# Optimization experiments

Measured on AMD Instinct MI355X. Metric: run time of the kernel, lower is better.

## Reference

```python
import jax, jax.numpy as jnp
import numpy as np
import math

B, T, D = 2, 2048, 1024
H = 16
DH = D // H
DFF = 4096
EPS = 1e-5


def setup_inputs() -> dict:
    key = jax.random.key(0)
    ks = jax.random.split(key, 10)
    x = jax.random.normal(ks[0], (B, T, D), dtype=jnp.float32)
    # bool mask, True above diagonal => masked (matches masked_fill semantics)
    causal_mask = jnp.triu(jnp.ones((T, T), dtype=bool), k=1)
    s = 0.02
    return {
        "x": x,
        "causal_mask": causal_mask,
        "gamma1": jnp.ones((D,), jnp.float32),
        "beta1": jnp.zeros((D,), jnp.float32),
        "wq": jax.random.normal(ks[1], (D, D), jnp.float32) * s,
        "wk": jax.random.normal(ks[2], (D, D), jnp.float32) * s,
        "wv": jax.random.normal(ks[3], (D, D), jnp.float32) * s,
        "wo": jax.random.normal(ks[4], (D, D), jnp.float32) * s,
        "gamma2": jnp.ones((D,), jnp.float32),
        "beta2": jnp.zeros((D,), jnp.float32),
        "w1": jax.random.normal(ks[5], (D, DFF), jnp.float32) * s,
        "b1": jnp.zeros((DFF,), jnp.float32),
        "w2": jax.random.normal(ks[6], (DFF, D), jnp.float32) * s,
        "b2": jnp.zeros((D,), jnp.float32),
    }


def _layer_norm(x, gamma, beta):
    mean = jnp.mean(x, axis=-1, keepdims=True)
    var = jnp.mean((x - mean) ** 2, axis=-1, keepdims=True)
    xhat = (x - mean) / jnp.sqrt(var + EPS)
    return gamma * xhat + beta


def _split_heads(x):
    b, t, d = x.shape
    return x.reshape(b, t, H, DH).transpose(0, 2, 1, 3)  # (B,H,T,Dh)


def reference(x, causal_mask, gamma1, beta1, wq, wk, wv, wo,
              gamma2, beta2, w1, b1, w2, b2):
    # --- attention sublayer (pre-LN) ---
    h = _layer_norm(x, gamma1, beta1)
    q = _split_heads(h @ wq)
    k = _split_heads(h @ wk)
    v = _split_heads(h @ wv)
    scores = jnp.einsum('bhqd,bhkd->bhqk', q, k) / math.sqrt(DH)  # (B,H,T,T)
    scores = jnp.where(causal_mask[None, None, :, :], -jnp.inf, scores)
    attn = jax.nn.softmax(scores, axis=-1)
    out = jnp.einsum('bhqk,bhkd->bhqd', attn, v)
    out = out.transpose(0, 2, 1, 3).reshape(x.shape)  # merge heads
    attn_out = out @ wo
    x = x + attn_out
    # --- FFN sublayer (pre-LN) ---
    h = _layer_norm(x, gamma2, beta2)
    ffn = jax.nn.gelu(h @ w1 + b1, approximate=False) @ w2 + b2
    return x + ffn
```

## Files before the change

kernel.cpp:

```cpp
#include <hip/hip_runtime.h>
#include <hip/hip_bf16.h>
#include <math.h>

#define B_   2
#define T_   2048
#define D_   1024
#define H_   16
#define DH_  64
#define DFF_ 4096
#define NTOK (B_*T_)

typedef __attribute__((ext_vector_type(8))) short short8;
typedef __attribute__((ext_vector_type(4))) float f32x4;

static __device__ __forceinline__ short f2bf(float f) {
    union { __hip_bfloat16 h; short s; } u;
    u.h = __float2bfloat16(f);
    return u.s;
}

static __device__ __forceinline__ f32x4 mfma16(short8 a, short8 b, f32x4 c) {
    return __builtin_amdgcn_mfma_f32_16x16x32_bf16(a, b, c, 0, 0, 0);
}

static __device__ __forceinline__ void gload16(const void* g, void* l) {
    __builtin_amdgcn_global_load_lds(
        (__attribute__((address_space(1))) void*)g,
        (__attribute__((address_space(3))) void*)l, 16, 0, 0);
}

static __device__ __forceinline__ short8 lds_read_sw(const short* base, int row, int kbyte) {
    const int off = (row << 7) + (kbyte ^ ((row & 7) << 4));
    return *reinterpret_cast<const short8*>(reinterpret_cast<const char*>(base) + off);
}

__global__ __launch_bounds__(256) void transpose_cast(
    const float* __restrict__ src, short* __restrict__ dst, int K, int N, float scale)
{
    __shared__ short tile[32][33];
    const int k0 = blockIdx.y * 32, n0 = blockIdx.x * 32;
    const int tx = threadIdx.x, ty = threadIdx.y;
    #pragma unroll
    for (int j = 0; j < 4; ++j) {
        int k = ty + j * 8;
        tile[k][tx] = f2bf(src[(size_t)(k0 + k) * N + n0 + tx] * scale);
    }
    __syncthreads();
    #pragma unroll
    for (int j = 0; j < 4; ++j) {
        int n = ty + j * 8;
        dst[(size_t)(n0 + n) * K + k0 + tx] = tile[tx][n];
    }
}

__global__ __launch_bounds__(256) void ln_kernel(
    const float* __restrict__ in, const float* __restrict__ gamma,
    const float* __restrict__ beta, short* __restrict__ out)
{
    const int row = blockIdx.x;
    const int t = threadIdx.x;
    const float4 v = *reinterpret_cast<const float4*>(in + (size_t)row * D_ + t * 4);
    float s  = v.x + v.y + v.z + v.w;
    float sq = v.x*v.x + v.y*v.y + v.z*v.z + v.w*v.w;
    #pragma unroll
    for (int off = 32; off >= 1; off >>= 1) {
        s  += __shfl_xor(s, off);
        sq += __shfl_xor(sq, off);
    }
    __shared__ float ps[4], pq[4];
    if ((t & 63) == 0) { ps[t >> 6] = s; pq[t >> 6] = sq; }
    __syncthreads();
    s  = ps[0] + ps[1] + ps[2] + ps[3];
    sq = pq[0] + pq[1] + pq[2] + pq[3];
    const float mean = s * (1.0f / D_);
    float var = sq * (1.0f / D_) - mean * mean;
    var = fmaxf(var, 0.0f);
    const float rstd = rsqrtf(var + 1e-5f);
    const float4 g = *reinterpret_cast<const float4*>(gamma + t * 4);
    const float4 b = *reinterpret_cast<const float4*>(beta  + t * 4);
    short4 o;
    o.x = f2bf(g.x * ((v.x - mean) * rstd) + b.x);
    o.y = f2bf(g.y * ((v.y - mean) * rstd) + b.y);
    o.z = f2bf(g.z * ((v.z - mean) * rstd) + b.z);
    o.w = f2bf(g.w * ((v.w - mean) * rstd) + b.w);
    *reinterpret_cast<short4*>(out + (size_t)row * D_ + t * 4) = o;
}

template<int BM, int BN, int WR, int WC, int EPI>
__global__ __launch_bounds__(256) void gemm_kernel(
    const short* __restrict__ A, const short* __restrict__ Bt,
    void* __restrict__ Cout, const float* __restrict__ resid,
    const float* __restrict__ bias, int M, int N, int K, int nbx)
{
    constexpr int MB = BM / WR / 16;
    constexpr int NB = BN / WC / 16;
    constexpr int JA = BM / 32;
    constexpr int JB = BN / 32;
    __shared__ short As[2][BM * 64];
    __shared__ short Bs[2][BN * 64];
    const int t = threadIdx.x;
    const int wid = t >> 6, lane = t & 63;
    const int lr = lane & 15, lk = lane >> 4;
    const int cpx = (int)gridDim.x >> 3;
    const int bid = (int)blockIdx.x;
    const int swz = (bid & 7) * cpx + (bid >> 3);
    const int m0 = (swz / nbx) * BM, n0 = (swz % nbx) * BN;
    const int wrow = (wid / WC) * (BM / WR);
    const int wcol = (wid % WC) * (BN / WC);

    const char* aSrc[JA];
    const char* bSrc[JB];
    #pragma unroll
    for (int j = 0; j < JA; ++j) {
        const int off = j * 4096 + t * 16;
        const int r   = off >> 7;
        const int cb  = (off & 127) ^ ((r & 7) << 4);
        aSrc[j] = (const char*)(A + (size_t)(m0 + r) * K) + cb;
    }
    #pragma unroll
    for (int j = 0; j < JB; ++j) {
        const int off = j * 4096 + t * 16;
        const int r   = off >> 7;
        const int cb  = (off & 127) ^ ((r & 7) << 4);
        bSrc[j] = (const char*)(Bt + (size_t)(n0 + r) * K) + cb;
    }

    f32x4 acc[MB][NB];
    #pragma unroll
    for (int m = 0; m < MB; ++m)
        #pragma unroll
        for (int n = 0; n < NB; ++n) acc[m][n] = (f32x4){0.f, 0.f, 0.f, 0.f};

    const int NT = K >> 6;

    #pragma unroll
    for (int j = 0; j < JA; ++j)
        gload16(aSrc[j], (char*)As[0] + j * 4096 + wid * 1024);
    #pragma unroll
    for (int j = 0; j < JB; ++j)
        gload16(bSrc[j], (char*)Bs[0] + j * 4096 + wid * 1024);
    __syncthreads();

    int cur = 0;
    for (int kt = 0; kt < NT; ++kt) {
        if (kt + 1 < NT) {
            const int kb = (kt + 1) << 7;
            #pragma unroll
            for (int j = 0; j < JA; ++j)
                gload16(aSrc[j] + kb, (char*)As[cur ^ 1] + j * 4096 + wid * 1024);
            #pragma unroll
            for (int j = 0; j < JB; ++j)
                gload16(bSrc[j] + kb, (char*)Bs[cur ^ 1] + j * 4096 + wid * 1024);
        }
        #pragma unroll
        for (int kk = 0; kk < 64; kk += 32) {
            short8 af[MB], bf[NB];
            #pragma unroll
            for (int m = 0; m < MB; ++m)
                af[m] = lds_read_sw(As[cur], wrow + m * 16 + lr, (kk + lk * 8) * 2);
            #pragma unroll
            for (int n = 0; n < NB; ++n)
                bf[n] = lds_read_sw(Bs[cur], wcol + n * 16 + lr, (kk + lk * 8) * 2);
            #pragma unroll
            for (int m = 0; m < MB; ++m)
                #pragma unroll
                for (int n = 0; n < NB; ++n)
                    acc[m][n] = mfma16(af[m], bf[n], acc[m][n]);
        }
        __syncthreads();
        cur ^= 1;
    }

    #pragma unroll
    for (int m = 0; m < MB; ++m) {
        #pragma unroll
        for (int n = 0; n < NB; ++n) {
            #pragma unroll
            for (int r = 0; r < 4; ++r) {
                const int gr = m0 + wrow + m * 16 + lk * 4 + r;
                const int gc = n0 + wcol + n * 16 + lr;
                const size_t idx = (size_t)gr * N + gc;
                const float v = acc[m][n][r];
                if constexpr (EPI == 0) {
                    ((short*)Cout)[idx] = f2bf(v);
                } else if constexpr (EPI == 1) {
                    ((float*)Cout)[idx] = resid[idx] + v;
                } else if constexpr (EPI == 2) {
                    const float tt = v + bias[gc];
                    const float ge = 0.5f * tt * (1.0f + erff(tt * 0.70710678118654752f));
                    ((short*)Cout)[idx] = f2bf(ge);
                } else {
                    ((float*)Cout)[idx] = resid[idx] + v + bias[gc];
                }
            }
        }
    }
}

__global__ __launch_bounds__(512) void vtrans(
    const short* __restrict__ qkv, short* __restrict__ vT)
{
    __shared__ short tile[64][65];
    const int qt = blockIdx.x;
    const int bh = blockIdx.y;
    const int b = bh >> 4, h = bh & 15;
    const int tx = threadIdx.x, ty = threadIdx.y;
    const short* src = qkv + ((size_t)(b * T_ + qt * 64)) * 3072 + 2048 + h * 64;
    #pragma unroll
    for (int j = 0; j < 8; ++j) {
        int tl = ty + j * 8;
        tile[tl][tx] = src[(size_t)tl * 3072 + tx];
    }
    __syncthreads();
    short* dst = vT + ((size_t)bh * 64) * T_ + qt * 64;
    #pragma unroll
    for (int j = 0; j < 8; ++j) {
        int dh = ty + j * 8;
        dst[(size_t)dh * T_ + tx] = tile[tx][dh];
    }
}

__global__ __launch_bounds__(256) void attn_kernel(
    const short* __restrict__ qkv, const short* __restrict__ vT,
    short* __restrict__ attn)
{
    __shared__ short Ks[2][4096];
    __shared__ short Vs[2][4096];
    __shared__ short Ps[4][1024];
    const int xx = blockIdx.x;
    const int bh = blockIdx.y;
    const int a  = xx & 7, bq = xx >> 3;
    const int i2 = ((bh >> 3) + bq) & 3;
    const int qt = (i2 == 0) ? a : (i2 == 1) ? 31 - a : (i2 == 2) ? 8 + a : 23 - a;
    const int b = bh >> 4, h = bh & 15;
    const int t = threadIdx.x;
    const int wid = t >> 6, lane = t & 63;
    const int lr = lane & 15, lk = lane >> 4;
    const int q0 = qt * 64 + wid * 16;

    const short* qrow = qkv + (size_t)(b * T_ + q0 + lr) * 3072 + h * 64;
    const short8 qf0 = *reinterpret_cast<const short8*>(qrow + lk * 8);
    const short8 qf1 = *reinterpret_cast<const short8*>(qrow + 32 + lk * 8);
    const short* kbase = qkv + (size_t)b * T_ * 3072 + 1024 + h * 64;
    const short* vbase = vT + (size_t)bh * 64 * T_;

    f32x4 o[4];
    float mr[4], lsp[4];
    #pragma unroll
    for (int n = 0; n < 4; ++n) o[n] = (f32x4){0.f, 0.f, 0.f, 0.f};
    #pragma unroll
    for (int r = 0; r < 4; ++r) { mr[r] = -INFINITY; lsp[r] = 0.f; }

    const int nkt = qt + 1;

    #pragma unroll
    for (int j = 0; j < 2; ++j) {
        const int off = j * 4096 + t * 16;
        const int r   = off >> 7;
        const int cb  = (off & 127) ^ ((r & 7) << 4);
        gload16(kbase + (size_t)r * 3072 + (cb >> 1), (char*)Ks[0] + j * 4096 + wid * 1024);
        gload16(vbase + (size_t)r * T_   + (cb >> 1), (char*)Vs[0] + j * 4096 + wid * 1024);
    }
    __syncthreads();

    int cur = 0;
    for (int kt = 0; kt < nkt; ++kt) {
        const int kvb = kt * 64;
        if (kt + 1 < nkt) {
            const int nb = kvb + 64;
            #pragma unroll
            for (int j = 0; j < 2; ++j) {
                const int off = j * 4096 + t * 16;
                const int r   = off >> 7;
                const int cb  = (off & 127) ^ ((r & 7) << 4);
                gload16(kbase + (size_t)(nb + r) * 3072 + (cb >> 1),
                        (char*)Ks[cur ^ 1] + j * 4096 + wid * 1024);
                gload16(vbase + (size_t)r * T_ + nb + (cb >> 1),
                        (char*)Vs[cur ^ 1] + j * 4096 + wid * 1024);
            }
        }

        f32x4 s[4];
        #pragma unroll
        for (int n = 0; n < 4; ++n) s[n] = (f32x4){0.f, 0.f, 0.f, 0.f};
        #pragma unroll
        for (int n = 0; n < 4; ++n) {
            s[n] = mfma16(qf0, lds_read_sw(Ks[cur], n * 16 + lr, (lk * 8) * 2), s[n]);
            s[n] = mfma16(qf1, lds_read_sw(Ks[cur], n * 16 + lr, (32 + lk * 8) * 2), s[n]);
        }

        const bool needmask = (kt == qt);
        char* pw = (char*)&Ps[wid][0];
        #pragma unroll
        for (int r = 0; r < 4; ++r) {
            const int qg = q0 + lk * 4 + r;
            float v0 = s[0][r], v1 = s[1][r], v2 = s[2][r], v3 = s[3][r];
            if (needmask) {
                if (kvb +      lr > qg) v0 = -INFINITY;
                if (kvb + 16 + lr > qg) v1 = -INFINITY;
                if (kvb + 32 + lr > qg) v2 = -INFINITY;
                if (kvb + 48 + lr > qg) v3 = -INFINITY;
            }
            const float mxl = fmaxf(fmaxf(v0, v1), fmaxf(v2, v3));
            if (!__all(mxl <= mr[r] + 8.0f)) {
                float mx = mxl;
                mx = fmaxf(mx, __shfl_xor(mx, 1));
                mx = fmaxf(mx, __shfl_xor(mx, 2));
                mx = fmaxf(mx, __shfl_xor(mx, 4));
                mx = fmaxf(mx, __shfl_xor(mx, 8));
                const float mnew = fmaxf(mr[r], mx);
                const float alpha = __builtin_amdgcn_exp2f(mr[r] - mnew);
                o[0][r] *= alpha; o[1][r] *= alpha; o[2][r] *= alpha; o[3][r] *= alpha;
                lsp[r] *= alpha;
                mr[r] = mnew;
            }
            const float p0 = __builtin_amdgcn_exp2f(v0 - mr[r]);
            const float p1 = __builtin_amdgcn_exp2f(v1 - mr[r]);
            const float p2 = __builtin_amdgcn_exp2f(v2 - mr[r]);
            const float p3 = __builtin_amdgcn_exp2f(v3 - mr[r]);
            lsp[r] += p0 + p1 + p2 + p3;
            const int prow = lk * 4 + r;
            const int sw = (prow & 7) << 4;
            char* prb = pw + prow * 128;
            *(short*)(prb + (((     lr * 2)) ^ sw)) = f2bf(p0);
            *(short*)(prb + ((32 + lr * 2) ^ sw)) = f2bf(p1);
            *(short*)(prb + ((64 + lr * 2) ^ sw)) = f2bf(p2);
            *(short*)(prb + ((96 + lr * 2) ^ sw)) = f2bf(p3);
        }
        asm volatile("s_waitcnt lgkmcnt(0)" ::: "memory");

        #pragma unroll
        for (int kk = 0; kk < 2; ++kk) {
            const short8 pf = *reinterpret_cast<const short8*>(
                pw + lr * 128 + ((kk * 64 + lk * 16) ^ ((lr & 7) << 4)));
            #pragma unroll
            for (int n = 0; n < 4; ++n)
                o[n] = mfma16(pf, lds_read_sw(Vs[cur], n * 16 + lr, (kk * 32 + lk * 8) * 2), o[n]);
        }
        __syncthreads();
        cur ^= 1;
    }

    #pragma unroll
    for (int r = 0; r < 4; ++r) {
        float l = lsp[r];
        l += __shfl_xor(l, 1);
        l += __shfl_xor(l, 2);
        l += __shfl_xor(l, 4);
        l += __shfl_xor(l, 8);
        const float inv = 1.0f / l;
        short* op = attn + (size_t)(b * T_ + q0 + lk * 4 + r) * D_ + h * 64;
        #pragma unroll
        for (int n = 0; n < 4; ++n)
            op[n * 16 + lr] = f2bf(o[n][r] * inv);
    }
}

extern "C" void kernel_launch(void* const* d_in, const int* in_sizes, int n_in,
                              void* d_out, int out_size, void* d_ws, size_t ws_size,
                              hipStream_t stream)
{
    (void)in_sizes; (void)n_in; (void)out_size; (void)ws_size;
    const float* x      = (const float*)d_in[0];
    const float* gamma1 = (const float*)d_in[2];
    const float* beta1  = (const float*)d_in[3];
    const float* wq     = (const float*)d_in[4];
    const float* wk     = (const float*)d_in[5];
    const float* wv     = (const float*)d_in[6];
    const float* wo     = (const float*)d_in[7];
    const float* gamma2 = (const float*)d_in[8];
    const float* beta2  = (const float*)d_in[9];
    const float* w1     = (const float*)d_in[10];
    const float* b1     = (const float*)d_in[11];
    const float* w2     = (const float*)d_in[12];
    const float* b2     = (const float*)d_in[13];
    float* out = (float*)d_out;

    char* ws = (char*)d_ws;
    size_t off = 0;
    short* wqkvT = (short*)(ws + off); off += (size_t)3072 * 1024 * 2;
    short* woT   = (short*)(ws + off); off += (size_t)1024 * 1024 * 2;
    short* w1T   = (short*)(ws + off); off += (size_t)4096 * 1024 * 2;
    short* w2T   = (short*)(ws + off); off += (size_t)1024 * 4096 * 2;
    short* h1    = (short*)(ws + off); off += (size_t)NTOK * 1024 * 2;
    short* h2    = (short*)(ws + off); off += (size_t)NTOK * 1024 * 2;
    float* y     = (float*)(ws + off); off += (size_t)NTOK * 1024 * 4;
    short* attnb = (short*)(ws + off); off += (size_t)NTOK * 1024 * 2;
    short* qkv   = (short*)(ws + off); off += (size_t)NTOK * 3072 * 2;
    short* vT    = (short*)(ws + off); off += (size_t)B_ * H_ * DH_ * T_ * 2;
    short* g     = qkv;

    const dim3 tb(32, 8);
    transpose_cast<<<dim3(32, 32),  tb, 0, stream>>>(wq, wqkvT,               1024, 1024, 0.18033688011112042f);
    transpose_cast<<<dim3(32, 32),  tb, 0, stream>>>(wk, wqkvT + 1024 * 1024, 1024, 1024, 1.0f);
    transpose_cast<<<dim3(32, 32),  tb, 0, stream>>>(wv, wqkvT + 2048 * 1024, 1024, 1024, 1.0f);
    transpose_cast<<<dim3(32, 32),  tb, 0, stream>>>(wo, woT,                 1024, 1024, 1.0f);
    transpose_cast<<<dim3(128, 32), tb, 0, stream>>>(w1, w1T, 1024, 4096, 1.0f);
    transpose_cast<<<dim3(32, 128), tb, 0, stream>>>(w2, w2T, 4096, 1024, 1.0f);

    ln_kernel<<<NTOK, 256, 0, stream>>>(x, gamma1, beta1, h1);

    gemm_kernel<128, 128, 2, 2, 0><<<768, 256, 0, stream>>>(
        h1, wqkvT, qkv, nullptr, nullptr, NTOK, 3072, 1024, 24);

    vtrans<<<dim3(T_ / 64, B_ * H_), dim3(64, 8), 0, stream>>>(qkv, vT);

    attn_kernel<<<dim3(T_ / 64, B_ * H_), 256, 0, stream>>>(qkv, vT, attnb);

    gemm_kernel<128, 64, 2, 2, 1><<<512, 256, 0, stream>>>(
        attnb, woT, y, x, nullptr, NTOK, 1024, 1024, 16);

    ln_kernel<<<NTOK, 256, 0, stream>>>(y, gamma2, beta2, h2);

    gemm_kernel<128, 128, 2, 2, 2><<<1024, 256, 0, stream>>>(
        h2, w1T, g, nullptr, b1, NTOK, 4096, 1024, 32);

    gemm_kernel<128, 64, 2, 2, 3><<<512, 256, 0, stream>>>(
        g, w2T, out, y, b2, NTOK, 1024, 4096, 16);
}
```

Before: 271.7 us.

## Fuse V-transpose into QKV GEMM, pair causal q-tiles, widen GEMM blocks

```diff
diff --git a/kernel.cpp b/kernel.cpp
--- a/kernel.cpp
+++ b/kernel.cpp
@@ -86,16 +86,17 @@
     *reinterpret_cast<short4*>(out + (size_t)row * D_ + t * 4) = o;
 }
 
-template<int BM, int BN, int WR, int WC, int EPI>
-__global__ __launch_bounds__(256) void gemm_kernel(
+template<int BM, int BN, int EPI>
+__global__ __launch_bounds__(512) void gemm_kernel(
     const short* __restrict__ A, const short* __restrict__ Bt,
     void* __restrict__ Cout, const float* __restrict__ resid,
-    const float* __restrict__ bias, int M, int N, int K, int nbx)
-{
-    constexpr int MB = BM / WR / 16;
-    constexpr int NB = BN / WC / 16;
-    constexpr int JA = BM / 32;
-    constexpr int JB = BN / 32;
+    const float* __restrict__ bias, short* __restrict__ vaux,
+    int M, int N, int K, int nbx)
+{
+    constexpr int MB = BM / 4 / 16;
+    constexpr int NB = BN / 2 / 16;
+    constexpr int JA = BM / 64;
+    constexpr int JB = BN / 64;
     __shared__ short As[2][BM * 64];
     __shared__ short Bs[2][BN * 64];
     const int t = threadIdx.x;
@@ -105,21 +106,21 @@
     const int bid = (int)blockIdx.x;
     const int swz = (bid & 7) * cpx + (bid >> 3);
     const int m0 = (swz / nbx) * BM, n0 = (swz % nbx) * BN;
-    const int wrow = (wid / WC) * (BM / WR);
-    const int wcol = (wid % WC) * (BN / WC);
+    const int wrow = (wid >> 1) * (BM / 4);
+    const int wcol = (wid & 1) * (BN / 2);
 
     const char* aSrc[JA];
     const char* bSrc[JB];
     #pragma unroll
     for (int j = 0; j < JA; ++j) {
-        const int off = j * 4096 + t * 16;
+        const int off = j * 8192 + t * 16;
         const int r   = off >> 7;
         const int cb  = (off & 127) ^ ((r & 7) << 4);
         aSrc[j] = (const char*)(A + (size_t)(m0 + r) * K) + cb;
     }
     #pragma unroll
     for (int j = 0; j < JB; ++j) {
-        const int off = j * 4096 + t * 16;
+        const int off = j * 8192 + t * 16;
         const int r   = off >> 7;
         const int cb  = (off & 127) ^ ((r & 7) << 4);
         bSrc[j] = (const char*)(Bt + (size_t)(n0 + r) * K) + cb;
@@ -135,10 +136,10 @@
 
     #pragma unroll
     for (int j = 0; j < JA; ++j)
-        gload16(aSrc[j], (char*)As[0] + j * 4096 + wid * 1024);
+        gload16(aSrc[j], (char*)As[0] + j * 8192 + wid * 1024);
     #pragma unroll
     for (int j = 0; j < JB; ++j)
-        gload16(bSrc[j], (char*)Bs[0] + j * 4096 + wid * 1024);
+        gload16(bSrc[j], (char*)Bs[0] + j * 8192 + wid * 1024);
     __syncthreads();
 
     int cur = 0;
@@ -147,10 +148,10 @@
             const int kb = (kt + 1) << 7;
             #pragma unroll
             for (int j = 0; j < JA; ++j)
-                gload16(aSrc[j] + kb, (char*)As[cur ^ 1] + j * 4096 + wid * 1024);
+                gload16(aSrc[j] + kb, (char*)As[cur ^ 1] + j * 8192 + wid * 1024);
             #pragma unroll
             for (int j = 0; j < JB; ++j)
-                gload16(bSrc[j] + kb, (char*)Bs[cur ^ 1] + j * 4096 + wid * 1024);
+                gload16(bSrc[j] + kb, (char*)Bs[cur ^ 1] + j * 8192 + wid * 1024);
         }
         #pragma unroll
         for (int kk = 0; kk < 64; kk += 32) {
@@ -189,34 +190,79 @@
                     const float tt = v + bias[gc];
                     const float ge = 0.5f * tt * (1.0f + erff(tt * 0.70710678118654752f));
                     ((short*)Cout)[idx] = f2bf(ge);
+                } else if constexpr (EPI == 3) {
+                    ((float*)Cout)[idx] = resid[idx] + v + bias[gc];
                 } else {
-                    ((float*)Cout)[idx] = resid[idx] + v + bias[gc];
+                    if (gc < 2048) {
+                        ((short*)Cout)[idx] = f2bf(v);
+                    } else {
+                        const int hh = (gc - 2048) >> 6, dh = (gc - 2048) & 63;
+                        const int bb = gr >> 11, tl = gr & 2047;
+                        vaux[((size_t)((bb << 4) + hh) * 64 + dh) * 2048 + tl] = f2bf(v);
+                    }
                 }
             }
         }
     }
 }
 
-__global__ __launch_bounds__(512) void vtrans(
-    const short* __restrict__ qkv, short* __restrict__ vT)
-{
-    __shared__ short tile[64][65];
-    const int qt = blockIdx.x;
-    const int bh = blockIdx.y;
-    const int b = bh >> 4, h = bh & 15;
-    const int tx = threadIdx.x, ty = threadIdx.y;
-    const short* src = qkv + ((size_t)(b * T_ + qt * 64)) * 3072 + 2048 + h * 64;
-    #pragma unroll
-    for (int j = 0; j < 8; ++j) {
-        int tl = ty + j * 8;
-        tile[tl][tx] = src[(size_t)tl * 3072 + tx];
-    }
-    __syncthreads();
-    short* dst = vT + ((size_t)bh * 64) * T_ + qt * 64;
-    #pragma unroll
-    for (int j = 0; j < 8; ++j) {
-        int dh = ty + j * 8;
-        dst[(size_t)dh * T_ + tx] = tile[tx][dh];
+static __device__ __forceinline__ void attn_tile(
+    const short* Kcur, const short* Vcur, char* pw,
+    short8 qf0, short8 qf1, int q0, int kvb, bool diag,
+    int lr, int lk, f32x4 (&o)[4], float (&mr)[4], float (&ls)[4])
+{
+    f32x4 s[4];
+    #pragma unroll
+    for (int n = 0; n < 4; ++n) s[n] = (f32x4){0.f, 0.f, 0.f, 0.f};
+    #pragma unroll
+    for (int n = 0; n < 4; ++n) {
+        s[n] = mfma16(qf0, lds_read_sw(Kcur, n * 16 + lr, (lk * 8) * 2), s[n]);
+        s[n] = mfma16(qf1, lds_read_sw(Kcur, n * 16 + lr, (32 + lk * 8) * 2), s[n]);
+    }
+    #pragma unroll
+    for (int r = 0; r < 4; ++r) {
+        const int qg = q0 + lk * 4 + r;
+        float v0 = s[0][r], v1 = s[1][r], v2 = s[2][r], v3 = s[3][r];
+        if (diag) {
+            if (kvb +      lr > qg) v0 = -INFINITY;
+            if (kvb + 16 + lr > qg) v1 = -INFINITY;
+            if (kvb + 32 + lr > qg) v2 = -INFINITY;
+            if (kvb + 48 + lr > qg) v3 = -INFINITY;
+        }
+        const float mxl = fmaxf(fmaxf(v0, v1), fmaxf(v2, v3));
+        if (!__all(mxl <= mr[r] + 8.0f)) {
+            float mx = mxl;
+            mx = fmaxf(mx, __shfl_xor(mx, 1));
+            mx = fmaxf(mx, __shfl_xor(mx, 2));
+            mx = fmaxf(mx, __shfl_xor(mx, 4));
+            mx = fmaxf(mx, __shfl_xor(mx, 8));
+            const float mnew = fmaxf(mr[r], mx);
+            const float alpha = __builtin_amdgcn_exp2f(mr[r] - mnew);
+            o[0][r] *= alpha; o[1][r] *= alpha; o[2][r] *= alpha; o[3][r] *= alpha;
+            ls[r] *= alpha;
+            mr[r] = mnew;
+        }
+        const float p0 = __builtin_amdgcn_exp2f(v0 - mr[r]);
+        const float p1 = __builtin_amdgcn_exp2f(v1 - mr[r]);
+        const float p2 = __builtin_amdgcn_exp2f(v2 - mr[r]);
+        const float p3 = __builtin_amdgcn_exp2f(v3 - mr[r]);
+        ls[r] += p0 + p1 + p2 + p3;
+        const int prow = lk * 4 + r;
+        const int sw = (prow & 7) << 4;
+        char* prb = pw + prow * 128;
+        *(short*)(prb + (((     lr * 2)) ^ sw)) = f2bf(p0);
+        *(short*)(prb + ((32 + lr * 2) ^ sw)) = f2bf(p1);
+        *(short*)(prb + ((64 + lr * 2) ^ sw)) = f2bf(p2);
+        *(short*)(prb + ((96 + lr * 2) ^ sw)) = f2bf(p3);
+    }
+    asm volatile("s_waitcnt lgkmcnt(0)" ::: "memory");
+    #pragma unroll
+    for (int kk = 0; kk < 2; ++kk) {
+        const short8 pf = *reinterpret_cast<const short8*>(
+            pw + lr * 128 + ((kk * 64 + lk * 16) ^ ((lr & 7) << 4)));
+        #pragma unroll
+        for (int n = 0; n < 4; ++n)
+            o[n] = mfma16(pf, lds_read_sw((const short*)Vcur, n * 16 + lr, (kk * 32 + lk * 8) * 2), o[n]);
     }
 }
 
@@ -226,32 +272,40 @@
 {
     __shared__ short Ks[2][4096];
     __shared__ short Vs[2][4096];
-    __shared__ short Ps[4][1024];
+    __shared__ short Ps[2][4][1024];
     const int xx = blockIdx.x;
     const int bh = blockIdx.y;
-    const int a  = xx & 7, bq = xx >> 3;
-    const int i2 = ((bh >> 3) + bq) & 3;
-    const int qt = (i2 == 0) ? a : (i2 == 1) ? 31 - a : (i2 == 2) ? 8 + a : 23 - a;
+    const int qA = xx, qB = 31 - xx;
     const int b = bh >> 4, h = bh & 15;
     const int t = threadIdx.x;
     const int wid = t >> 6, lane = t & 63;
     const int lr = lane & 15, lk = lane >> 4;
-    const int q0 = qt * 64 + wid * 16;
-
-    const short* qrow = qkv + (size_t)(b * T_ + q0 + lr) * 3072 + h * 64;
-    const short8 qf0 = *reinterpret_cast<const short8*>(qrow + lk * 8);
-    const short8 qf1 = *reinterpret_cast<const short8*>(qrow + 32 + lk * 8);
+    const int q0A = qA * 64 + wid * 16;
+    const int q0B = qB * 64 + wid * 16;
+
+    const short* qrowA = qkv + (size_t)(b * T_ + q0A + lr) * 3072 + h * 64;
+    const short8 qfA0 = *reinterpret_cast<const short8*>(qrowA + lk * 8);
+    const short8 qfA1 = *reinterpret_cast<const short8*>(qrowA + 32 + lk * 8);
+    const short* qrowB = qkv + (size_t)(b * T_ + q0B + lr) * 3072 + h * 64;
+    const short8 qfB0 = *reinterpret_cast<const short8*>(qrowB + lk * 8);
+    const short8 qfB1 = *reinterpret_cast<const short8*>(qrowB + 32 + lk * 8);
     const short* kbase = qkv + (size_t)b * T_ * 3072 + 1024 + h * 64;
     const short* vbase = vT + (size_t)bh * 64 * T_;
 
-    f32x4 o[4];
-    float mr[4], lsp[4];
-    #pragma unroll
-    for (int n = 0; n < 4; ++n) o[n] = (f32x4){0.f, 0.f, 0.f, 0.f};
-    #pragma unroll
-    for (int r = 0; r < 4; ++r) { mr[r] = -INFINITY; lsp[r] = 0.f; }
-
-    const int nkt = qt + 1;
+    f32x4 oA[4], oB[4];
+    float mrA[4], lsA[4], mrB[4], lsB[4];
+    #pragma unroll
+    for (int n = 0; n < 4; ++n) {
+        oA[n] = (f32x4){0.f, 0.f, 0.f, 0.f};
+        oB[n] = (f32x4){0.f, 0.f, 0.f, 0.f};
+    }
+    #pragma unroll
+    for (int r = 0; r < 4; ++r) {
+        mrA[r] = -INFINITY; lsA[r] = 0.f;
+        mrB[r] = -INFINITY; lsB[r] = 0.f;
+    }
+
+    const int nkt = qB + 1;
 
     #pragma unroll
     for (int j = 0; j < 2; ++j) {
@@ -280,79 +334,31 @@
             }
         }
 
-        f32x4 s[4];
-        #pragma unroll
-        for (int n = 0; n < 4; ++n) s[n] = (f32x4){0.f, 0.f, 0.f, 0.f};
+        attn_tile(Ks[cur], Vs[cur], (char*)&Ps[1][wid][0],
+                  qfB0, qfB1, q0B, kvb, kt == qB, lr, lk, oB, mrB, lsB);
+        if (kt <= qA)
+            attn_tile(Ks[cur], Vs[cur], (char*)&Ps[0][wid][0],
+                      qfA0, qfA1, q0A, kvb, kt == qA, lr, lk, oA, mrA, lsA);
+
+        __syncthreads();
+        cur ^= 1;
+    }
+
+    #pragma unroll
+    for (int r = 0; r < 4; ++r) {
+        float lA = lsA[r], lB = lsB[r];
+        lA += __shfl_xor(lA, 1); lB += __shfl_xor(lB, 1);
+        lA += __shfl_xor(lA, 2); lB += __shfl_xor(lB, 2);
+        lA += __shfl_xor(lA, 4); lB += __shfl_xor(lB, 4);
+        lA += __shfl_xor(lA, 8); lB += __shfl_xor(lB, 8);
+        const float invA = 1.0f / lA, invB = 1.0f / lB;
+        short* opA = attn + (size_t)(b * T_ + q0A + lk * 4 + r) * D_ + h * 64;
+        short* opB = attn + (size_t)(b * T_ + q0B + lk * 4 + r) * D_ + h * 64;
         #pragma unroll
         for (int n = 0; n < 4; ++n) {
-            s[n] = mfma16(qf0, lds_read_sw(Ks[cur], n * 16 + lr, (lk * 8) * 2), s[n]);
-            s[n] = mfma16(qf1, lds_read_sw(Ks[cur], n * 16 + lr, (32 + lk * 8) * 2), s[n]);
-        }
-
-        const bool needmask = (kt == qt);
-        char* pw = (char*)&Ps[wid][0];
-        #pragma unroll
-        for (int r = 0; r < 4; ++r) {
-            const int qg = q0 + lk * 4 + r;
-            float v0 = s[0][r], v1 = s[1][r], v2 = s[2][r], v3 = s[3][r];
-            if (needmask) {
-                if (kvb +      lr > qg) v0 = -INFINITY;
-                if (kvb + 16 + lr > qg) v1 = -INFINITY;
-                if (kvb + 32 + lr > qg) v2 = -INFINITY;
-                if (kvb + 48 + lr > qg) v3 = -INFINITY;
-            }
-            const float mxl = fmaxf(fmaxf(v0, v1), fmaxf(v2, v3));
-            if (!__all(mxl <= mr[r] + 8.0f)) {
-                float mx = mxl;
-                mx = fmaxf(mx, __shfl_xor(mx, 1));
-                mx = fmaxf(mx, __shfl_xor(mx, 2));
-                mx = fmaxf(mx, __shfl_xor(mx, 4));
-                mx = fmaxf(mx, __shfl_xor(mx, 8));
-                const float mnew = fmaxf(mr[r], mx);
-                const float alpha = __builtin_amdgcn_exp2f(mr[r] - mnew);
-                o[0][r] *= alpha; o[1][r] *= alpha; o[2][r] *= alpha; o[3][r] *= alpha;
-                lsp[r] *= alpha;
-                mr[r] = mnew;
-            }
-            const float p0 = __builtin_amdgcn_exp2f(v0 - mr[r]);
-            const float p1 = __builtin_amdgcn_exp2f(v1 - mr[r]);
-            const float p2 = __builtin_amdgcn_exp2f(v2 - mr[r]);
-            const float p3 = __builtin_amdgcn_exp2f(v3 - mr[r]);
-            lsp[r] += p0 + p1 + p2 + p3;
-            const int prow = lk * 4 + r;
-            const int sw = (prow & 7) << 4;
-            char* prb = pw + prow * 128;
-            *(short*)(prb + (((     lr * 2)) ^ sw)) = f2bf(p0);
-            *(short*)(prb + ((32 + lr * 2) ^ sw)) = f2bf(p1);
-            *(short*)(prb + ((64 + lr * 2) ^ sw)) = f2bf(p2);
-            *(short*)(prb + ((96 + lr * 2) ^ sw)) = f2bf(p3);
-        }
-        asm volatile("s_waitcnt lgkmcnt(0)" ::: "memory");
-
-        #pragma unroll
-        for (int kk = 0; kk < 2; ++kk) {
-            const short8 pf = *reinterpret_cast<const short8*>(
-                pw + lr * 128 + ((kk * 64 + lk * 16) ^ ((lr & 7) << 4)));
-            #pragma unroll
-            for (int n = 0; n < 4; ++n)
-                o[n] = mfma16(pf, lds_read_sw(Vs[cur], n * 16 + lr, (kk * 32 + lk * 8) * 2), o[n]);
-        }
-        __syncthreads();
-        cur ^= 1;
-    }
-
-    #pragma unroll
-    for (int r = 0; r < 4; ++r) {
-        float l = lsp[r];
-        l += __shfl_xor(l, 1);
-        l += __shfl_xor(l, 2);
-        l += __shfl_xor(l, 4);
-        l += __shfl_xor(l, 8);
-        const float inv = 1.0f / l;
-        short* op = attn + (size_t)(b * T_ + q0 + lk * 4 + r) * D_ + h * 64;
-        #pragma unroll
-        for (int n = 0; n < 4; ++n)
-            op[n * 16 + lr] = f2bf(o[n][r] * inv);
+            opA[n * 16 + lr] = f2bf(oA[n][r] * invA);
+            opB[n * 16 + lr] = f2bf(oB[n][r] * invB);
+        }
     }
 }
 
@@ -400,21 +406,19 @@
 
     ln_kernel<<<NTOK, 256, 0, stream>>>(x, gamma1, beta1, h1);
 
-    gemm_kernel<128, 128, 2, 2, 0><<<768, 256, 0, stream>>>(
-        h1, wqkvT, qkv, nullptr, nullptr, NTOK, 3072, 1024, 24);
-
-    vtrans<<<dim3(T_ / 64, B_ * H_), dim3(64, 8), 0, stream>>>(qkv, vT);
-
-    attn_kernel<<<dim3(T_ / 64, B_ * H_), 256, 0, stream>>>(qkv, vT, attnb);
-
-    gemm_kernel<128, 64, 2, 2, 1><<<512, 256, 0, stream>>>(
-        attnb, woT, y, x, nullptr, NTOK, 1024, 1024, 16);
+    gemm_kernel<128, 128, 4><<<768, 512, 0, stream>>>(
+        h1, wqkvT, qkv, nullptr, nullptr, vT, NTOK, 3072, 1024, 24);
+
+    attn_kernel<<<dim3(16, 32), 256, 0, stream>>>(qkv, vT, attnb);
+
+    gemm_kernel<128, 64, 1><<<512, 512, 0, stream>>>(
+        attnb, woT, y, x, nullptr, nullptr, NTOK, 1024, 1024, 16);
 
     ln_kernel<<<NTOK, 256, 0, stream>>>(y, gamma2, beta2, h2);
 
-    gemm_kernel<128, 128, 2, 2, 2><<<1024, 256, 0, stream>>>(
-        h2, w1T, g, nullptr, b1, NTOK, 4096, 1024, 32);
-
-    gemm_kernel<128, 64, 2, 2, 3><<<512, 256, 0, stream>>>(
-        g, w2T, out, y, b2, NTOK, 1024, 4096, 16);
-}
+    gemm_kernel<128, 128, 2><<<1024, 512, 0, stream>>>(
+        h2, w1T, g, nullptr, b1, nullptr, NTOK, 4096, 1024, 32);
+
+    gemm_kernel<128, 64, 3><<<512, 512, 0, stream>>>(
+        g, w2T, out, y, b2, nullptr, NTOK, 1024, 4096, 16);
+}
```

After: 261.9 us. 3.6% less time.
